# Performance work log

Measured on AMD Instinct MI355X. Metric: run time of the kernel, lower is better.

The kernel has to match this reference:

```python
import jax, jax.numpy as jnp
import numpy as np

BITS = (2, 4, 6, 8, 12, 16)
INIT_S = (0.5, 0.1, 0.05, 0.01, 0.005, 0.001)


def _round_ste(x):
    # straight-through round (LSQ)
    return x + jax.lax.stop_gradient(jnp.round(x) - x)


def _grad_scale(s, g):
    # forward = s, backward grad scaled by g (LSQ grad-scale trick)
    return s * g + jax.lax.stop_gradient(s - s * g)


def _lsq(x, s, num_bits):
    qn = -(2 ** (num_bits - 1))
    qp = 2 ** (num_bits - 1) - 1
    g = 1.0 / float(np.sqrt(x.size * qp))
    ss = _grad_scale(s, g)
    return _round_ste(jnp.clip(x / ss, qn, qp)) * ss


def _gumbel_hard(key, logits, tau):
    u = jax.random.uniform(key, logits.shape, minval=1e-10, maxval=1.0)
    gn = -jnp.log(-jnp.log(u))
    y_soft = jax.nn.softmax((logits + gn) / tau, axis=-1)
    y_hard = jax.nn.one_hot(jnp.argmax(y_soft, axis=-1), logits.shape[-1], dtype=y_soft.dtype)
    return y_hard + y_soft - jax.lax.stop_gradient(y_soft)


def setup_inputs() -> dict:
    key = jax.random.key(0)
    ks = jax.random.split(key, 16)
    B, L, N, K, HD = 64, 256, 8, 64, 64
    inp = {
        "v": jax.random.normal(ks[0], (B, L, K, 2), jnp.float32),
        "H": jax.random.normal(ks[1], (B, L, N, K, 2), jnp.float32),
        "y": jax.random.normal(ks[2], (B, L, N, 2), jnp.float32),
        "local_snr": jax.random.uniform(ks[3], (B, L, K, 1), jnp.float32),
        "w1": jax.random.normal(ks[4], (HD, 9), jnp.float32) * 0.05,
        "b1": jnp.zeros((HD,), jnp.float32),
        "w2": jax.random.normal(ks[5], (HD, HD), jnp.float32) * 0.05,
        "b2": jnp.zeros((HD,), jnp.float32),
        "w3": jax.random.normal(ks[6], (HD, HD), jnp.float32) * 0.05,
        "b3": jnp.zeros((HD,), jnp.float32),
        "wy": jax.random.normal(ks[7], (6, HD), jnp.float32) * 0.05,
        "by": jnp.zeros((6,), jnp.float32),
        "wh": jax.random.normal(ks[8], (6, HD), jnp.float32) * 0.05,
        "bh": jnp.zeros((6,), jnp.float32),
        "wd": jax.random.normal(ks[9], (6, HD), jnp.float32) * 0.05,
        "bd": jnp.zeros((6,), jnp.float32),
        "s_y": jnp.asarray(INIT_S, jnp.float32),
        "s_H": jnp.asarray(INIT_S, jnp.float32),
        "s_d": jnp.asarray(INIT_S, jnp.float32),
        "tau": 1,
    }
    return inp


def reference(v, H, y, local_snr, w1, b1, w2, b2, w3, b3, wy, by, wh, bh, wd, bd, s_y, s_H, s_d, tau):
    tau = float(tau)
    B, L, K, _ = v.shape
    N = H.shape[2]

    v_real = v[..., 0:1]
    v_imag = v[..., 1:2]
    h_power = (H ** 2).sum(axis=(2, 4))                       # (B,L,K)
    channel_norm = h_power[..., None]
    avg_channel_power = jnp.broadcast_to(h_power.mean(axis=1, keepdims=True), (B, L, K))[..., None]
    total_power = h_power.sum(axis=2, keepdims=True)          # (B,L,1)
    interference = total_power - h_power
    sir = jnp.log1p(h_power / (interference + 1e-10))[..., None]
    total_power_norm = jnp.broadcast_to(jnp.log1p(total_power), (B, L, K))[..., None]
    y_power_per_ap = (y ** 2).sum(axis=(2, 3))                # (B,L)
    y_power = jnp.broadcast_to(jnp.log1p(y_power_per_ap)[:, :, None, None], (B, L, K, 1))
    signal_power = jnp.sqrt(v_real ** 2 + v_imag ** 2 + 1e-10)

    feat = jnp.concatenate([v_real, v_imag, local_snr, channel_norm, avg_channel_power,
                            sir, total_power_norm, y_power, signal_power], axis=-1)  # (B,L,K,9)

    h = jax.nn.relu(feat @ w1.T + b1)
    h = jax.nn.relu(h @ w2.T + b2)
    h = jax.nn.relu(h @ w3.T + b3)
    logits_y = h @ wy.T + by
    logits_H = h @ wh.T + bh
    logits_d = h @ wd.T + bd

    logits_y_per_ap = logits_y.mean(axis=2)                   # (B,L,6)
    gkey = jax.random.key(42)
    g1, g2, g3 = jax.random.split(gkey, 3)
    w_y = _gumbel_hard(g1, logits_y_per_ap, tau)              # (B,L,6)
    w_H = _gumbel_hard(g2, logits_H, tau)                     # (B,L,K,6)
    w_demod = _gumbel_hard(g3, logits_d, tau)                 # (B,L,K,6)

    y_stack = jnp.stack([_lsq(y, s_y[i], BITS[i]) for i in range(6)], axis=2)   # (B,L,6,N,2)
    y_q = (y_stack * w_y[:, :, :, None, None]).sum(axis=2)

    H_stack = jnp.stack([_lsq(H, s_H[i], BITS[i]) for i in range(6)], axis=4)   # (B,L,N,K,6,2)
    H_q = (H_stack * w_H[:, :, None, :, :, None]).sum(axis=4)

    v_stack = jnp.stack([_lsq(v, s_d[i], BITS[i]) for i in range(6)], axis=3)   # (B,L,K,6,2)
    v_q = (v_stack * w_demod[..., None]).sum(axis=3)

    bit_values = jnp.asarray([2.0, 4.0, 6.0, 8.0, 12.0, 16.0], v.dtype)
    y_bits_per_ap = 2.0 * N * (w_y * bit_values).sum(axis=-1)                   # (B,L)
    y_bits_per_link = y_bits_per_ap[..., None] / K
    H_bits_per_link = 2.0 * N * (w_H * bit_values).sum(axis=-1)                 # (B,L,K)
    demod_bits_per_link = 2.0 * (w_demod * bit_values).sum(axis=-1)             # (B,L,K)
    expected_bits = y_bits_per_link + H_bits_per_link + demod_bits_per_link

    return (v_q, H_q, y_q, expected_bits, w_y, w_H, w_demod,
            y_bits_per_ap, H_bits_per_link, demod_bits_per_link)
```

## Files before the change

### kernel.cpp

```cpp
#include <hip/hip_runtime.h>
#include <cstdint>


#define JAX_PARTITIONABLE 1

constexpr int BL = 64 * 256;

constexpr long long O_vq  = 0;
constexpr long long O_Hq  = 2097152;
constexpr long long O_yq  = 18874368;
constexpr long long O_eb  = 19136512;
constexpr long long O_wy  = 20185088;
constexpr long long O_wH  = 20283392;
constexpr long long O_wd  = 26574848;
constexpr long long O_yba = 32866304;
constexpr long long O_Hbl = 32882688;
constexpr long long O_dbl = 33931264;

constexpr long long F_SAMPLE = 0;
constexpr long long F_M      = 1048576;

#define MARGIN_THETA 3e-4

__device__ __forceinline__ uint32_t rotl32(uint32_t v, int d) {
// ... 58 lines not shown
  for (int off = 32; off > 0; off >>= 1) x += __shfl_xor(x, off);
  return x;
}

__device__ __forceinline__ void argmax_gap6(const double* s, int& arg, double& gap) {
  int a = 0;
#pragma unroll
  for (int j = 1; j < 6; ++j) if (s[j] > s[a]) a = j;
  double second = -1e300;
#pragma unroll
  for (int j = 0; j < 6; ++j) if (j != a && s[j] > second) second = s[j];
  arg = a; gap = s[a] - second;
}

__device__ __forceinline__ float idx_to_bits(int i) {
  return (float)((i < 4) ? 2 * (i + 1) : (i == 4 ? 12 : 16));
}

__global__ void k0_setup(const float* __restrict__ sy, const float* __restrict__ sH,
                         const float* __restrict__ sd, float* __restrict__ ss,
                         uint32_t* __restrict__ keys) {
  const int t = threadIdx.x;
  if (t < 18) {
    const int tensor = t / 6, i = t % 6;
    const int qp_[6] = {1, 7, 31, 127, 2047, 32767};
    const long long sizes[3] = {262144LL, 16777216LL, 2097152LL};
    const float* sarr = tensor == 0 ? sy : (tensor == 1 ? sH : sd);
    const double g64 = 1.0 / sqrt((double)(sizes[tensor] * (long long)qp_[i]));
    const float g32 = (float)g64;
    const float s = sarr[i];
    const float t1 = s * g32;
    ss[t] = t1 + (s - t1);
  }
#if JAX_PARTITIONABLE
  if (t >= 32 && t < 35) {
    uint32_t o0, o1;
    threefry2x32(0u, 42u, 0u, (uint32_t)(t - 32), o0, o1);
    keys[(t - 32) * 2 + 0] = o0;
    keys[(t - 32) * 2 + 1] = o1;
  }
#else
  if (t == 32) {
    uint32_t a0, b0, a1, b1, a2, b2;
    threefry2x32(0u, 42u, 0u, 3u, a0, b0);
    threefry2x32(0u, 42u, 1u, 4u, a1, b1);
    threefry2x32(0u, 42u, 2u, 5u, a2, b2);
    keys[0] = a0; keys[1] = a1;
    keys[2] = a2; keys[3] = b0;
    keys[4] = b1; keys[5] = b2;
  }
#endif
}

__global__ __launch_bounds__(128) void k1a_hpower_partial(
    const float* __restrict__ Hm, double* __restrict__ partial) {
  const int blk = blockIdx.x;
  const int b = blk >> 3, lc = blk & 7;
  const int t = threadIdx.x;
  const float* base = Hm + (size_t)(b * 256 + lc * 32) * 1024;
  double acc = 0.0;
  for (int l = 0; l < 32; ++l) {
#pragma unroll
    for (int n = 0; n < 8; ++n) {
      const float x = base[(size_t)l * 1024 + n * 128 + t];
      acc = fma((double)x, (double)x, acc);
    }
  }
  const double other = __shfl_xor(acc, 1);
  if ((t & 1) == 0) partial[(size_t)blk * 64 + (t >> 1)] = acc + other;
}

__global__ void k1b_hpmean(const double* __restrict__ partial,
                           double* __restrict__ hp_mean) {
  const int id = blockIdx.x * blockDim.x + threadIdx.x;
  if (id >= 4096) return;
  const int b = id >> 6, k = id & 63;
  double s = 0.0;
#pragma unroll
  for (int lc = 0; lc < 8; ++lc) s += partial[(size_t)(b * 8 + lc) * 64 + k];
  hp_mean[id] = s * (1.0 / 256.0);
}

template <int NI, bool RELU>
__device__ __forceinline__ void gemm64(const float* __restrict__ inT,
                                       const float* __restrict__ WT,
                                       const float* __restrict__ bias,
                                       float* __restrict__ outT, int t) {
  const int k0 = (t & 15) * 4;
  const int j0 = (t >> 4) * 4;
  float acc[16];
#pragma unroll
  for (int jj = 0; jj < 4; ++jj) {
    const float bj = bias[j0 + jj];
#pragma unroll
    for (int kk = 0; kk < 4; ++kk) acc[jj * 4 + kk] = bj;
  }
#pragma unroll 16
  for (int i = 0; i < NI; ++i) {
    const float4 x  = *(const float4*)&inT[i * 68 + k0];
    const float4 wv = *(const float4*)&WT[i * 64 + j0];
    acc[0]  = fmaf(wv.x, x.x, acc[0]);
    acc[1]  = fmaf(wv.x, x.y, acc[1]);
    acc[2]  = fmaf(wv.x, x.z, acc[2]);
    acc[3]  = fmaf(wv.x, x.w, acc[3]);
    acc[4]  = fmaf(wv.y, x.x, acc[4]);
    acc[5]  = fmaf(wv.y, x.y, acc[5]);
    acc[6]  = fmaf(wv.y, x.z, acc[6]);
    acc[7]  = fmaf(wv.y, x.w, acc[7]);
    acc[8]  = fmaf(wv.z, x.x, acc[8]);
    acc[9]  = fmaf(wv.z, x.y, acc[9]);
    acc[10] = fmaf(wv.z, x.z, acc[10]);
    acc[11] = fmaf(wv.z, x.w, acc[11]);
    acc[12] = fmaf(wv.w, x.x, acc[12]);
    acc[13] = fmaf(wv.w, x.y, acc[13]);
    acc[14] = fmaf(wv.w, x.z, acc[14]);
    acc[15] = fmaf(wv.w, x.w, acc[15]);
  }
#pragma unroll
  for (int jj = 0; jj < 4; ++jj) {
    float4 r;
    r.x = acc[jj * 4 + 0];
    r.y = acc[jj * 4 + 1];
    r.z = acc[jj * 4 + 2];
    r.w = acc[jj * 4 + 3];
    if (RELU) {
      r.x = fmaxf(r.x, 0.0f); r.y = fmaxf(r.y, 0.0f);
      r.z = fmaxf(r.z, 0.0f); r.w = fmaxf(r.w, 0.0f);
    }
    *(float4*)&outT[(j0 + jj) * 68 + k0] = r;
  }
}

template <int NI>
__device__ __forceinline__ void gemm64_f64(const double* __restrict__ inT,
                                           const float* __restrict__ WT,
                                           const float* __restrict__ bias,
                                           double* __restrict__ outT, int t) {
  const int k0 = (t & 15) * 4;
  const int j0 = (t >> 4) * 4;
  double acc[16];
#pragma unroll
  for (int jj = 0; jj < 4; ++jj) {
    const double bj = (double)bias[j0 + jj];
#pragma unroll
    for (int kk = 0; kk < 4; ++kk) acc[jj * 4 + kk] = bj;
  }
#pragma unroll 8
  for (int i = 0; i < NI; ++i) {
    const double x0 = inT[i * 68 + k0 + 0];
    const double x1 = inT[i * 68 + k0 + 1];
    const double x2 = inT[i * 68 + k0 + 2];
    const double x3 = inT[i * 68 + k0 + 3];
    const float4 wf = *(const float4*)&WT[i * 64 + j0];
    const double w0 = (double)wf.x, w1 = (double)wf.y;
    const double w2 = (double)wf.z, w3 = (double)wf.w;
    acc[0]  = fma(w0, x0, acc[0]);
    acc[1]  = fma(w0, x1, acc[1]);
    acc[2]  = fma(w0, x2, acc[2]);
    acc[3]  = fma(w0, x3, acc[3]);
    acc[4]  = fma(w1, x0, acc[4]);
    acc[5]  = fma(w1, x1, acc[5]);
    acc[6]  = fma(w1, x2, acc[6]);
    acc[7]  = fma(w1, x3, acc[7]);
    acc[8]  = fma(w2, x0, acc[8]);
    acc[9]  = fma(w2, x1, acc[9]);
    acc[10] = fma(w2, x2, acc[10]);
    acc[11] = fma(w2, x3, acc[11]);
    acc[12] = fma(w3, x0, acc[12]);
    acc[13] = fma(w3, x1, acc[13]);
    acc[14] = fma(w3, x2, acc[14]);
    acc[15] = fma(w3, x3, acc[15]);
  }
#pragma unroll
  for (int jj = 0; jj < 4; ++jj) {
#pragma unroll
    for (int kk = 0; kk < 4; ++kk) {
      const double a = acc[jj * 4 + kk];
      outT[(j0 + jj) * 68 + k0 + kk] = a > 0.0 ? a : 0.0;
    }
  }
}

__device__ __forceinline__ void heads20(const float* __restrict__ actT,
                                        const float* __restrict__ whT,
                                        const float* __restrict__ by,
                                        const float* __restrict__ bh,
                                        const float* __restrict__ bd,
                                        float* __restrict__ headP, int t) {
  const int k = t & 63, w = t >> 6;
  float acc[5];
#pragma unroll
  for (int q = 0; q < 5; ++q) {
    const int r = w + 4 * q;
    acc[q] = (r < 6) ? by[r] : (r < 12) ? bh[r - 6] : (r < 18) ? bd[r - 12] : 0.0f;
  }
#pragma unroll 8
  for (int i = 0; i < 64; ++i) {
    const float x = actT[i * 68 + k];
#pragma unroll
    for (int q = 0; q < 5; ++q)
      acc[q] = fmaf(x, whT[(w + 4 * q) * 64 + i], acc[q]);
  }
#pragma unroll
  for (int q = 0; q < 5; ++q) {
    const int r = w + 4 * q;
    if (r < 18) headP[k * 20 + r] = acc[q];
  }
}

__device__ __forceinline__ void heads20_f64(const double* __restrict__ actT,
                                            const float* __restrict__ whT,
                                            const float* __restrict__ by,
                                            const float* __restrict__ bh,
                                            const float* __restrict__ bd,
                                            double* __restrict__ headP, int t) {
  const int k = t & 63, w = t >> 6;
  double acc[5];
#pragma unroll
  for (int q = 0; q < 5; ++q) {
    const int r = w + 4 * q;
    acc[q] = (r < 6) ? (double)by[r]
           : (r < 12) ? (double)bh[r - 6]
           : (r < 18) ? (double)bd[r - 12] : 0.0;
  }
#pragma unroll 8
  for (int i = 0; i < 64; ++i) {
    const double x = actT[i * 68 + k];
#pragma unroll
    for (int q = 0; q < 5; ++q)
      acc[q] = fma(x, (double)whT[(w + 4 * q) * 64 + i], acc[q]);
  }
#pragma unroll
  for (int q = 0; q < 5; ++q) {
    const int r = w + 4 * q;
    if (r < 18) headP[k * 20 + r] = acc[q];
  }
}

__global__ __launch_bounds__(256, 2) void k2_main(
    const float* __restrict__ v, const float* __restrict__ Hm,
    const float* __restrict__ y, const float* __restrict__ snr,
    const float* __restrict__ w1, const float* __restrict__ b1,
    const float* __restrict__ w2, const float* __restrict__ b2,
    const float* __restrict__ w3, const float* __restrict__ b3,
    const float* __restrict__ wy, const float* __restrict__ by,
    const float* __restrict__ wh, const float* __restrict__ bh,
    const float* __restrict__ wd, const float* __restrict__ bd,
    const double* __restrict__ hp_mean, const uint32_t* __restrict__ keys,
    float* __restrict__ out) {
  const int t = threadIdx.x;
  const int lane = t & 63;
  const int wvx = t >> 6;
  const int m0 = blockIdx.x * 4;

  __shared__ __align__(16) float smem[20032];
  float* w1T   = smem;
  float* w2T   = smem + 576;
  float* w3T   = smem + 4672;
  float* whT   = smem + 8768;
  float* actA  = smem + 10048;
  float* actB  = smem + 14400;
  float* headP = smem + 18752;
  double* hp4  = (double*)actB;

  for (int idx = t; idx < 576; idx += 256) {
    const int i = idx >> 6, j = idx & 63;
    w1T[idx] = w1[j * 9 + i];
  }
  for (int idx = t; idx < 4096; idx += 256) {
    const int i = idx >> 6, j = idx & 63;
    w2T[idx] = w2[j * 64 + i];
    w3T[idx] = w3[j * 64 + i];
  }
  for (int idx = t; idx < 1280; idx += 256) {
    const int r = idx >> 6, i = idx & 63;
    whT[idx] = (r < 6) ? wy[r * 64 + i]
             : (r < 12) ? wh[(r - 6) * 64 + i]
             : (r < 18) ? wd[(r - 12) * 64 + i] : 0.0f;
  }

  float ly[6], lh[6], ld[6];
#pragma unroll 1
  for (int mc = 0; mc < 4; ++mc) {
    const int m = m0 + mc;
    {
      const float2* Hp = (const float2*)Hm + (size_t)m * 512;
      double acc = 0.0;
#pragma unroll
      for (int nn = 0; nn < 2; ++nn) {
        const float2 h2v = Hp[(2 * wvx + nn) * 64 + lane];
        acc = fma((double)h2v.x, (double)h2v.x, acc);
        acc = fma((double)h2v.y, (double)h2v.y, acc);
      }
      __syncthreads();
      hp4[wvx * 64 + lane] = acc;
    }
    __syncthreads();

    if (wvx == mc) {
      const double hp = ((hp4[lane] + hp4[64 + lane]) + hp4[128 + lane]) + hp4[192 + lane];
      const double tp = wave_sum_f64(hp);
      double ypart = 0.0;
      if (lane < 16) { const double yv = (double)y[m * 16 + lane]; ypart = yv * yv; }
      const double yp = wave_sum_f64(ypart);
      const float2 vv = ((const float2*)v)[m * 64 + lane];
      const float snrv = snr[m * 64 + lane];
      const double hpm = hp_mean[(m >> 8) * 64 + lane];
      float f[9];
      f[0] = (float)vv.x;
      f[1] = (float)vv.y;
      f[2] = snrv;
      f[3] = (float)hp;
      f[4] = (float)hpm;
      f[5] = (float)log1p(hp / ((tp - hp) + 1e-10));
      f[6] = (float)log1p(tp);
      f[7] = (float)log1p(yp);
      f[8] = (float)sqrt(fma((double)vv.x, (double)vv.x,
                             fma((double)vv.y, (double)vv.y, 1e-10)));
#pragma unroll
      for (int i = 0; i < 9; ++i) actA[i * 68 + lane] = f[i];
    }
    __syncthreads();

    gemm64<9, true>(actA, w1T, b1, actB, t);
    __syncthreads();
    gemm64<64, true>(actB, w2T, b2, actA, t);
    __syncthreads();
    gemm64<64, true>(actA, w3T, b3, actB, t);
    __syncthreads();
    heads20(actB, whT, by, bh, bd, headP, t);
    __syncthreads();

    if (wvx == mc) {
#pragma unroll
      for (int j = 0; j < 6; ++j) {
        ly[j] = headP[lane * 20 + j];
        lh[j] = headP[lane * 20 + 6 + j];
        ld[j] = headP[lane * 20 + 12 + j];
      }
    }
  }

  const int m = m0 + wvx;
  const int k = lane;

  const uint32_t g1k0 = keys[0], g1k1 = keys[1];
  const uint32_t g2k0 = keys[2], g2k1 = keys[3];
  const uint32_t g3k0 = keys[4], g3k1 = keys[5];

  double sH[6], sD[6];
  const uint32_t eH = (uint32_t)(m * 64 + k) * 6u;
#pragma unroll
  for (int j = 0; j < 6; ++j) {
    const float u = bits_to_unif(jax_randbits(g2k0, g2k1, eH + j, 6291456u));
    sH[j] = (double)lh[j] + (double)(-logf(-logf(u)));
  }
#pragma unroll
  for (int j = 0; j < 6; ++j) {
    const float u = bits_to_unif(jax_randbits(g3k0, g3k1, eH + j, 6291456u));
    sD[j] = (double)ld[j] + (double)(-logf(-logf(u)));
  }
  int argH, argD; double gapH, gapD;
  argmax_gap6(sH, argH, gapH);
  argmax_gap6(sD, argD, gapD);

  double lysum[6];
#pragma unroll
  for (int j = 0; j < 6; ++j) lysum[j] = wave_sum_f64((double)ly[j]);

  int argY = 0; double gapY = 1e30;
  if (k == 0) {
    double sY[6];
#pragma unroll
    for (int j = 0; j < 6; ++j) {
      const float u = bits_to_unif(jax_randbits(g1k0, g1k1, (uint32_t)(m * 6 + j), 98304u));
      sY[j] = lysum[j] * (1.0 / 64.0) - log(-log((double)u));
    }
    argmax_gap6(sY, argY, gapY);
  }
  const int needY = __shfl((k == 0 && gapY < MARGIN_THETA) ? 1 : 0, 0);
  const bool fH = gapH < MARGIN_THETA;
  const bool fD = gapD < MARGIN_THETA;

  uint8_t* flags = (uint8_t*)(out + O_vq);
  flags[F_SAMPLE + (size_t)m * 64 + k] = (uint8_t)((fH ? 1 : 0) | (fD ? 2 : 0));
  const bool anyHD = __ballot(fH || fD) != 0ull;
  if (k == 0)
    flags[F_M + m] = (uint8_t)(((anyHD || needY) ? 1 : 0) | (needY ? 2 : 0));

  argY = __shfl(argY, 0);

  const float bY = 16.0f * idx_to_bits(argY);
  const float bH = 16.0f * idx_to_bits(argH);
  const float bD = 2.0f * idx_to_bits(argD);

  if (k == 0) {
    out[O_yba + m] = bY;
#pragma unroll
    for (int j = 0; j < 6; ++j) out[O_wy + m * 6 + j] = (j == argY) ? 1.0f : 0.0f;
  }
  out[O_Hbl + (size_t)m * 64 + k] = bH;
  out[O_dbl + (size_t)m * 64 + k] = bD;
  out[O_eb + (size_t)m * 64 + k] = (bY * 0.015625f + bH) + bD;
#pragma unroll
  for (int j = 0; j < 6; ++j) {
    out[O_wH + (size_t)(m * 64 + k) * 6 + j] = (j == argH) ? 1.0f : 0.0f;
    out[O_wd + (size_t)(m * 64 + k) * 6 + j] = (j == argD) ? 1.0f : 0.0f;
  }
}

__global__ __launch_bounds__(256, 1) void kfix(
    const float* __restrict__ v, const float* __restrict__ Hm,
    const float* __restrict__ y, const float* __restrict__ snr,
    const float* __restrict__ w1, const float* __restrict__ b1,
    const float* __restrict__ w2, const float* __restrict__ b2,
    const float* __restrict__ w3, const float* __restrict__ b3,
    const float* __restrict__ wy, const float* __restrict__ by,
    const float* __restrict__ wh, const float* __restrict__ bh,
    const float* __restrict__ wd, const float* __restrict__ bd,
    const double* __restrict__ hp_mean, const uint32_t* __restrict__ keys,
    float* __restrict__ out) {
  const int t = threadIdx.x;
  const int lane = t & 63;
  const int wvx = t >> 6;
  const int m0 = blockIdx.x * 8;
  const uint8_t* flags = (const uint8_t*)(out + O_vq);

  __shared__ uint32_t mfs[8];
  __shared__ __align__(32) char smem[120064];
  float*  w1T     = (float*)smem;
  float*  w2T     = (float*)(smem + 2304);
  float*  w3T     = (float*)(smem + 18688);
  float*  whT     = (float*)(smem + 35072);
  double* actA64  = (double*)(smem + 40192);
  double* actB64  = (double*)(smem + 75008);
  double* headP64 = (double*)(smem + 109824);
  double* hp4     = actB64;

  if (t < 8) mfs[t] = flags[F_M + m0 + t];
  __syncthreads();
  bool any = false;
#pragma unroll
  for (int i = 0; i < 8; ++i) any |= (mfs[i] != 0);
  if (!any) return;

  for (int idx = t; idx < 576; idx += 256) {
    const int i = idx >> 6, j = idx & 63;
    w1T[idx] = w1[j * 9 + i];
  }
  for (int idx = t; idx < 4096; idx += 256) {
    const int i = idx >> 6, j = idx & 63;
    w2T[idx] = w2[j * 64 + i];
    w3T[idx] = w3[j * 64 + i];
  }
  for (int idx = t; idx < 1280; idx += 256) {
    const int r = idx >> 6, i = idx & 63;
    whT[idx] = (r < 6) ? wy[r * 64 + i]
             : (r < 12) ? wh[(r - 6) * 64 + i]
             : (r < 18) ? wd[(r - 12) * 64 + i] : 0.0f;
  }
// ... 174 lines not shown
  float2 o;
  o.x = lsq1(x.x, ssv, qn, qp);
  o.y = lsq1(x.y, ssv, qn, qp);
  ((float2*)outvq)[id] = o;
}

__global__ void k5_yq(const float* __restrict__ y, const float* __restrict__ ss,
                      const float* __restrict__ ybits, float* __restrict__ outyq) {
  const int id = blockIdx.x * blockDim.x + threadIdx.x;
  if (id >= 131072) return;
  const int m = id >> 3;
  const int bits = (int)ybits[m] >> 4;
  const int i = bits_to_idx(bits);
  const float ssv = ss[i];
  const float qp = (float)((1 << (bits - 1)) - 1);
  const float qn = -(float)(1 << (bits - 1));
  const float2 x = ((const float2*)y)[id];
  float2 o;
  o.x = lsq1(x.x, ssv, qn, qp);
  o.y = lsq1(x.y, ssv, qn, qp);
  ((float2*)outyq)[id] = o;
}

extern "C" void kernel_launch(void* const* d_in, const int* in_sizes, int n_in,
                              void* d_out, int out_size, void* d_ws, size_t ws_size,
                              hipStream_t stream) {
  const float* v   = (const float*)d_in[0];
  const float* Hm  = (const float*)d_in[1];
  const float* y   = (const float*)d_in[2];
  const float* snr = (const float*)d_in[3];
  const float* w1  = (const float*)d_in[4];
  const float* b1  = (const float*)d_in[5];
  const float* w2  = (const float*)d_in[6];
  const float* b2  = (const float*)d_in[7];
  const float* w3  = (const float*)d_in[8];
  const float* b3  = (const float*)d_in[9];
  const float* wy  = (const float*)d_in[10];
  const float* by  = (const float*)d_in[11];
  const float* wh  = (const float*)d_in[12];
  const float* bh  = (const float*)d_in[13];
  const float* wd  = (const float*)d_in[14];
  const float* bd  = (const float*)d_in[15];
  const float* sy  = (const float*)d_in[16];
  const float* sH  = (const float*)d_in[17];
  const float* sd  = (const float*)d_in[18];

  float* out = (float*)d_out;

  double* ws_partial = (double*)d_ws;
  double* ws_hpmean  = ws_partial + 32768;
  float*  ws_ss      = (float*)(ws_hpmean + 4096);
  uint32_t* ws_keys  = (uint32_t*)(ws_ss + 18);

  k0_setup<<<1, 64, 0, stream>>>(sy, sH, sd, ws_ss, ws_keys);
  k1a_hpower_partial<<<512, 128, 0, stream>>>(Hm, ws_partial);
  k1b_hpmean<<<16, 256, 0, stream>>>(ws_partial, ws_hpmean);
  k2_main<<<BL / 4, 256, 0, stream>>>(v, Hm, y, snr, w1, b1, w2, b2, w3, b3,
                                      wy, by, wh, bh, wd, bd, ws_hpmean, ws_keys, out);
  kfix<<<BL / 8, 256, 0, stream>>>(v, Hm, y, snr, w1, b1, w2, b2, w3, b3,
                                   wy, by, wh, bh, wd, bd, ws_hpmean, ws_keys, out);
  k3_Hq<<<32768, 256, 0, stream>>>(Hm, ws_ss, out + O_Hbl, out + O_Hq);
  k4_vq<<<4096, 256, 0, stream>>>(v, ws_ss, out + O_dbl, out + O_vq);
  k5_yq<<<512, 256, 0, stream>>>(y, ws_ss, out + O_yba, out + O_yq);
}
```

Measured before the change: 857.6 us.

## Pre-transpose MLP weights once and run one sample per k2 block

A new small kernel transposes all MLP and head weights into a scratch area (the H_q output region, which k3 overwrites later), so k2_main no longer rebuilds a 40 KB shared-memory weight copy in every block. k2_main now handles one sample per block instead of four, reads weights from global/L2, computes each GEMM layer into registers and writes back in place to a single activation buffer. The launch bound is raised to 4 blocks per CU, cutting LDS use to about 22 KB per block. This removes redundant per-block weight staging and improves occupancy, at the cost of 4x more blocks, weight reads through cache instead of LDS, and three idle waves during the tail sampling stage.

```diff
diff --git a/kernel.cpp b/kernel.cpp
--- a/kernel.cpp
+++ b/kernel.cpp
@@ -134,6 +134,25 @@
 #endif
 }
 
+__global__ void k0w_transpose(const float* __restrict__ w1, const float* __restrict__ w2,
+                              const float* __restrict__ w3, const float* __restrict__ wy,
+                              const float* __restrict__ wh, const float* __restrict__ wd,
+                              float* __restrict__ wsT) {
+  const int t = blockIdx.x * blockDim.x + threadIdx.x;
+  for (int idx = t; idx < 576; idx += 4096)
+    wsT[idx] = w1[(idx & 63) * 9 + (idx >> 6)];
+  for (int idx = t; idx < 4096; idx += 4096) {
+    wsT[576 + idx]  = w2[(idx & 63) * 64 + (idx >> 6)];
+    wsT[4672 + idx] = w3[(idx & 63) * 64 + (idx >> 6)];
+  }
+  for (int idx = t; idx < 1280; idx += 4096) {
+    const int r = idx >> 6, i = idx & 63;
+    wsT[8768 + idx] = (r < 6) ? wy[r * 64 + i]
+                    : (r < 12) ? wh[(r - 6) * 64 + i]
+                    : (r < 18) ? wd[(r - 12) * 64 + i] : 0.0f;
+  }
+}
+
 __global__ __launch_bounds__(128) void k1a_hpower_partial(
     const float* __restrict__ Hm, double* __restrict__ partial) {
   const int blk = blockIdx.x;
@@ -163,14 +182,13 @@
   hp_mean[id] = s * (1.0 / 256.0);
 }
 
-template <int NI, bool RELU>
-__device__ __forceinline__ void gemm64(const float* __restrict__ inT,
-                                       const float* __restrict__ WT,
-                                       const float* __restrict__ bias,
-                                       float* __restrict__ outT, int t) {
+template <int NI>
+__device__ __forceinline__ void gemm_acc(const float* inT,
+                                         const float* __restrict__ WT,
+                                         const float* __restrict__ bias,
+                                         float* acc, int t) {
   const int k0 = (t & 15) * 4;
   const int j0 = (t >> 4) * 4;
-  float acc[16];
 #pragma unroll
   for (int jj = 0; jj < 4; ++jj) {
     const float bj = bias[j0 + jj];
@@ -198,18 +216,202 @@
     acc[14] = fmaf(wv.w, x.z, acc[14]);
     acc[15] = fmaf(wv.w, x.w, acc[15]);
   }
+}
+
+__device__ __forceinline__ void gemm_store(const float* acc, float* outT, int t) {
+  const int k0 = (t & 15) * 4;
+  const int j0 = (t >> 4) * 4;
 #pragma unroll
   for (int jj = 0; jj < 4; ++jj) {
     float4 r;
-    r.x = acc[jj * 4 + 0];
-    r.y = acc[jj * 4 + 1];
-    r.z = acc[jj * 4 + 2];
-    r.w = acc[jj * 4 + 3];
-    if (RELU) {
-      r.x = fmaxf(r.x, 0.0f); r.y = fmaxf(r.y, 0.0f);
-      r.z = fmaxf(r.z, 0.0f); r.w = fmaxf(r.w, 0.0f);
+    r.x = fmaxf(acc[jj * 4 + 0], 0.0f);
+    r.y = fmaxf(acc[jj * 4 + 1], 0.0f);
+    r.z = fmaxf(acc[jj * 4 + 2], 0.0f);
+    r.w = fmaxf(acc[jj * 4 + 3], 0.0f);
+    *(float4*)&outT[(j0 + jj) * 68 + k0] = r;
+  }
+}
+
+__device__ __forceinline__ void heads20(const float* actT,
+                                        const float* __restrict__ whT,
+                                        const float* __restrict__ by,
+                                        const float* __restrict__ bh,
+                                        const float* __restrict__ bd,
+                                        float* headP, int t) {
+  const int k = t & 63, w = t >> 6;
+  float acc[5];
+#pragma unroll
+  for (int q = 0; q < 5; ++q) {
+    const int r = w + 4 * q;
+    acc[q] = (r < 6) ? by[r] : (r < 12) ? bh[r - 6] : (r < 18) ? bd[r - 12] : 0.0f;
+  }
+#pragma unroll 8
+  for (int i = 0; i < 64; ++i) {
+    const float x = actT[i * 68 + k];
+#pragma unroll
+    for (int q = 0; q < 5; ++q)
+      acc[q] = fmaf(x, whT[(w + 4 * q) * 64 + i], acc[q]);
+  }
+#pragma unroll
+  for (int q = 0; q < 5; ++q) {
+    const int r = w + 4 * q;
+    if (r < 18) headP[k * 20 + r] = acc[q];
+  }
+}
+
+__global__ __launch_bounds__(256, 4) void k2_main(
+    const float* __restrict__ v, const float* __restrict__ Hm,
+    const float* __restrict__ y, const float* __restrict__ snr,
+    const float* __restrict__ b1, const float* __restrict__ b2,
+    const float* __restrict__ b3, const float* __restrict__ by,
+    const float* __restrict__ bh, const float* __restrict__ bd,
+    const float* __restrict__ wsT, const double* __restrict__ hp_mean,
+    const uint32_t* __restrict__ keys, float* __restrict__ out) {
+  const int t = threadIdx.x;
+  const int lane = t & 63;
+  const int wvx = t >> 6;
+  const int m = blockIdx.x;
+
+  __shared__ __align__(16) float smem[5632];
+  float* act   = smem;
+  float* headP = smem + 4352;
+  double* hp4  = (double*)headP;
+
+  {
+    const float2* Hp = (const float2*)Hm + (size_t)m * 512;
+    double acc = 0.0;
+#pragma unroll
+    for (int nn = 0; nn < 2; ++nn) {
+      const float2 h2v = Hp[(2 * wvx + nn) * 64 + lane];
+      acc = fma((double)h2v.x, (double)h2v.x, acc);
+      acc = fma((double)h2v.y, (double)h2v.y, acc);
     }
-    *(float4*)&outT[(j0 + jj) * 68 + k0] = r;
+    hp4[wvx * 64 + lane] = acc;
+  }
+  __syncthreads();
+
+  if (wvx == 0) {
+    const double hp = ((hp4[lane] + hp4[64 + lane]) + hp4[128 + lane]) + hp4[192 + lane];
+    const double tp = wave_sum_f64(hp);
+    double ypart = 0.0;
+    if (lane < 16) { const double yv = (double)y[m * 16 + lane]; ypart = yv * yv; }
+    const double yp = wave_sum_f64(ypart);
+    const float2 vv = ((const float2*)v)[m * 64 + lane];
+    const float snrv = snr[m * 64 + lane];
+    const double hpm = hp_mean[(m >> 8) * 64 + lane];
+    float f[9];
+    f[0] = (float)vv.x;
+    f[1] = (float)vv.y;
+    f[2] = snrv;
+    f[3] = (float)hp;
+    f[4] = (float)hpm;
+    f[5] = (float)log1p(hp / ((tp - hp) + 1e-10));
+    f[6] = (float)log1p(tp);
+    f[7] = (float)log1p(yp);
+    f[8] = (float)sqrt(fma((double)vv.x, (double)vv.x,
+                           fma((double)vv.y, (double)vv.y, 1e-10)));
+#pragma unroll
+    for (int i = 0; i < 9; ++i) act[i * 68 + lane] = f[i];
+  }
+  __syncthreads();
+
+  {
+    float a1[16];
+    gemm_acc<9>(act, wsT, b1, a1, t);
+    __syncthreads();
+    gemm_store(a1, act, t);
+  }
+  __syncthreads();
+  {
+    float a2[16];
+    gemm_acc<64>(act, wsT + 576, b2, a2, t);
+    __syncthreads();
+    gemm_store(a2, act, t);
+  }
+  __syncthreads();
+  {
+    float a3[16];
+    gemm_acc<64>(act, wsT + 4672, b3, a3, t);
+    __syncthreads();
+    gemm_store(a3, act, t);
+  }
+  __syncthreads();
+  heads20(act, wsT + 8768, by, bh, bd, headP, t);
+  __syncthreads();
+
+  if (wvx != 0) return;
+
+  const int k = lane;
+  float ly[6], lh[6], ld[6];
+#pragma unroll
+  for (int j = 0; j < 6; ++j) {
+    ly[j] = headP[k * 20 + j];
+    lh[j] = headP[k * 20 + 6 + j];
+    ld[j] = headP[k * 20 + 12 + j];
+  }
+
+  const uint32_t g1k0 = keys[0], g1k1 = keys[1];
+  const uint32_t g2k0 = keys[2], g2k1 = keys[3];
+  const uint32_t g3k0 = keys[4], g3k1 = keys[5];
+
+  double sH[6], sD[6];
+  const uint32_t eH = (uint32_t)(m * 64 + k) * 6u;
+#pragma unroll
+  for (int j = 0; j < 6; ++j) {
+    const float u = bits_to_unif(jax_randbits(g2k0, g2k1, eH + j, 6291456u));
+    sH[j] = (double)lh[j] + (double)(-logf(-logf(u)));
+  }
+#pragma unroll
+  for (int j = 0; j < 6; ++j) {
+    const float u = bits_to_unif(jax_randbits(g3k0, g3k1, eH + j, 6291456u));
+    sD[j] = (double)ld[j] + (double)(-logf(-logf(u)));
+  }
+  int argH, argD; double gapH, gapD;
+  argmax_gap6(sH, argH, gapH);
+  argmax_gap6(sD, argD, gapD);
+
+  double lysum[6];
+#pragma unroll
+  for (int j = 0; j < 6; ++j) lysum[j] = wave_sum_f64((double)ly[j]);
+
+  int argY = 0; double gapY = 1e30;
+  if (k == 0) {
+    double sY[6];
+#pragma unroll
+    for (int j = 0; j < 6; ++j) {
+      const float u = bits_to_unif(jax_randbits(g1k0, g1k1, (uint32_t)(m * 6 + j), 98304u));
+      sY[j] = lysum[j] * (1.0 / 64.0) - log(-log((double)u));
+    }
+    argmax_gap6(sY, argY, gapY);
+  }
+  const int needY = __shfl((k == 0 && gapY < MARGIN_THETA) ? 1 : 0, 0);
+  const bool fH = gapH < MARGIN_THETA;
+  const bool fD = gapD < MARGIN_THETA;
+
+  uint8_t* flags = (uint8_t*)(out + O_vq);
+  flags[F_SAMPLE + (size_t)m * 64 + k] = (uint8_t)((fH ? 1 : 0) | (fD ? 2 : 0));
+  const bool anyHD = __ballot(fH || fD) != 0ull;
+  if (k == 0)
+    flags[F_M + m] = (uint8_t)(((anyHD || needY) ? 1 : 0) | (needY ? 2 : 0));
+
+  argY = __shfl(argY, 0);
+
+  const float bY = 16.0f * idx_to_bits(argY);
+  const float bH = 16.0f * idx_to_bits(argH);
+  const float bD = 2.0f * idx_to_bits(argD);
+
+  if (k == 0) {
+    out[O_yba + m] = bY;
+#pragma unroll
+    for (int j = 0; j < 6; ++j) out[O_wy + m * 6 + j] = (j == argY) ? 1.0f : 0.0f;
+  }
+  out[O_Hbl + (size_t)m * 64 + k] = bH;
+  out[O_dbl + (size_t)m * 64 + k] = bD;
+  out[O_eb + (size_t)m * 64 + k] = (bY * 0.015625f + bH) + bD;
+#pragma unroll
+  for (int j = 0; j < 6; ++j) {
+    out[O_wH + (size_t)(m * 64 + k) * 6 + j] = (j == argH) ? 1.0f : 0.0f;
+    out[O_wd + (size_t)(m * 64 + k) * 6 + j] = (j == argD) ? 1.0f : 0.0f;
   }
 }
 
@@ -263,33 +465,6 @@
   }
 }
 
-__device__ __forceinline__ void heads20(const float* __restrict__ actT,
-                                        const float* __restrict__ whT,
-                                        const float* __restrict__ by,
-                                        const float* __restrict__ bh,
-                                        const float* __restrict__ bd,
-                                        float* __restrict__ headP, int t) {
-  const int k = t & 63, w = t >> 6;
-  float acc[5];
-#pragma unroll
-  for (int q = 0; q < 5; ++q) {
-    const int r = w + 4 * q;
-    acc[q] = (r < 6) ? by[r] : (r < 12) ? bh[r - 6] : (r < 18) ? bd[r - 12] : 0.0f;
-  }
-#pragma unroll 8
-  for (int i = 0; i < 64; ++i) {
-    const float x = actT[i * 68 + k];
-#pragma unroll
-    for (int q = 0; q < 5; ++q)
-      acc[q] = fmaf(x, whT[(w + 4 * q) * 64 + i], acc[q]);
-  }
-#pragma unroll
-  for (int q = 0; q < 5; ++q) {
-    const int r = w + 4 * q;
-    if (r < 18) headP[k * 20 + r] = acc[q];
-  }
-}
-
 __device__ __forceinline__ void heads20_f64(const double* __restrict__ actT,
                                             const float* __restrict__ whT,
                                             const float* __restrict__ by,
@@ -316,178 +491,6 @@
   for (int q = 0; q < 5; ++q) {
     const int r = w + 4 * q;
     if (r < 18) headP[k * 20 + r] = acc[q];
-  }
-}
-
-__global__ __launch_bounds__(256, 2) void k2_main(
-    const float* __restrict__ v, const float* __restrict__ Hm,
-    const float* __restrict__ y, const float* __restrict__ snr,
-    const float* __restrict__ w1, const float* __restrict__ b1,
-    const float* __restrict__ w2, const float* __restrict__ b2,
-    const float* __restrict__ w3, const float* __restrict__ b3,
-    const float* __restrict__ wy, const float* __restrict__ by,
-    const float* __restrict__ wh, const float* __restrict__ bh,
-    const float* __restrict__ wd, const float* __restrict__ bd,
-    const double* __restrict__ hp_mean, const uint32_t* __restrict__ keys,
-    float* __restrict__ out) {
-  const int t = threadIdx.x;
-  const int lane = t & 63;
-  const int wvx = t >> 6;
-  const int m0 = blockIdx.x * 4;
-
-  __shared__ __align__(16) float smem[20032];
-  float* w1T   = smem;
-  float* w2T   = smem + 576;
-  float* w3T   = smem + 4672;
-  float* whT   = smem + 8768;
-  float* actA  = smem + 10048;
-  float* actB  = smem + 14400;
-  float* headP = smem + 18752;
-  double* hp4  = (double*)actB;
-
-  for (int idx = t; idx < 576; idx += 256) {
-    const int i = idx >> 6, j = idx & 63;
-    w1T[idx] = w1[j * 9 + i];
-  }
-  for (int idx = t; idx < 4096; idx += 256) {
-    const int i = idx >> 6, j = idx & 63;
-    w2T[idx] = w2[j * 64 + i];
-    w3T[idx] = w3[j * 64 + i];
-  }
-  for (int idx = t; idx < 1280; idx += 256) {
-    const int r = idx >> 6, i = idx & 63;
-    whT[idx] = (r < 6) ? wy[r * 64 + i]
-             : (r < 12) ? wh[(r - 6) * 64 + i]
-             : (r < 18) ? wd[(r - 12) * 64 + i] : 0.0f;
-  }
-
-  float ly[6], lh[6], ld[6];
-#pragma unroll 1
-  for (int mc = 0; mc < 4; ++mc) {
-    const int m = m0 + mc;
-    {
-      const float2* Hp = (const float2*)Hm + (size_t)m * 512;
-      double acc = 0.0;
-#pragma unroll
-      for (int nn = 0; nn < 2; ++nn) {
-        const float2 h2v = Hp[(2 * wvx + nn) * 64 + lane];
-        acc = fma((double)h2v.x, (double)h2v.x, acc);
-        acc = fma((double)h2v.y, (double)h2v.y, acc);
-      }
-      __syncthreads();
-      hp4[wvx * 64 + lane] = acc;
-    }
-    __syncthreads();
-
-    if (wvx == mc) {
-      const double hp = ((hp4[lane] + hp4[64 + lane]) + hp4[128 + lane]) + hp4[192 + lane];
-      const double tp = wave_sum_f64(hp);
-      double ypart = 0.0;
-      if (lane < 16) { const double yv = (double)y[m * 16 + lane]; ypart = yv * yv; }
-      const double yp = wave_sum_f64(ypart);
-      const float2 vv = ((const float2*)v)[m * 64 + lane];
-      const float snrv = snr[m * 64 + lane];
-      const double hpm = hp_mean[(m >> 8) * 64 + lane];
-      float f[9];
-      f[0] = (float)vv.x;
-      f[1] = (float)vv.y;
-      f[2] = snrv;
-      f[3] = (float)hp;
-      f[4] = (float)hpm;
-      f[5] = (float)log1p(hp / ((tp - hp) + 1e-10));
-      f[6] = (float)log1p(tp);
-      f[7] = (float)log1p(yp);
-      f[8] = (float)sqrt(fma((double)vv.x, (double)vv.x,
-                             fma((double)vv.y, (double)vv.y, 1e-10)));
-#pragma unroll
-      for (int i = 0; i < 9; ++i) actA[i * 68 + lane] = f[i];
-    }
-    __syncthreads();
-
-    gemm64<9, true>(actA, w1T, b1, actB, t);
-    __syncthreads();
-    gemm64<64, true>(actB, w2T, b2, actA, t);
-    __syncthreads();
-    gemm64<64, true>(actA, w3T, b3, actB, t);
-    __syncthreads();
-    heads20(actB, whT, by, bh, bd, headP, t);
-    __syncthreads();
-
-    if (wvx == mc) {
-#pragma unroll
-      for (int j = 0; j < 6; ++j) {
-        ly[j] = headP[lane * 20 + j];
-        lh[j] = headP[lane * 20 + 6 + j];
-        ld[j] = headP[lane * 20 + 12 + j];
-      }
-    }
-  }
-
-  const int m = m0 + wvx;
-  const int k = lane;
-
-  const uint32_t g1k0 = keys[0], g1k1 = keys[1];
-  const uint32_t g2k0 = keys[2], g2k1 = keys[3];
-  const uint32_t g3k0 = keys[4], g3k1 = keys[5];
-
-  double sH[6], sD[6];
-  const uint32_t eH = (uint32_t)(m * 64 + k) * 6u;
-#pragma unroll
-  for (int j = 0; j < 6; ++j) {
-    const float u = bits_to_unif(jax_randbits(g2k0, g2k1, eH + j, 6291456u));
-    sH[j] = (double)lh[j] + (double)(-logf(-logf(u)));
-  }
-#pragma unroll
-  for (int j = 0; j < 6; ++j) {
-    const float u = bits_to_unif(jax_randbits(g3k0, g3k1, eH + j, 6291456u));
-    sD[j] = (double)ld[j] + (double)(-logf(-logf(u)));
-  }
-  int argH, argD; double gapH, gapD;
-  argmax_gap6(sH, argH, gapH);
-  argmax_gap6(sD, argD, gapD);
-
-  double lysum[6];
-#pragma unroll
-  for (int j = 0; j < 6; ++j) lysum[j] = wave_sum_f64((double)ly[j]);
-
-  int argY = 0; double gapY = 1e30;
-  if (k == 0) {
-    double sY[6];
-#pragma unroll
-    for (int j = 0; j < 6; ++j) {
-      const float u = bits_to_unif(jax_randbits(g1k0, g1k1, (uint32_t)(m * 6 + j), 98304u));
-      sY[j] = lysum[j] * (1.0 / 64.0) - log(-log((double)u));
-    }
-    argmax_gap6(sY, argY, gapY);
-  }
-  const int needY = __shfl((k == 0 && gapY < MARGIN_THETA) ? 1 : 0, 0);
-  const bool fH = gapH < MARGIN_THETA;
-  const bool fD = gapD < MARGIN_THETA;
-
-  uint8_t* flags = (uint8_t*)(out + O_vq);
-  flags[F_SAMPLE + (size_t)m * 64 + k] = (uint8_t)((fH ? 1 : 0) | (fD ? 2 : 0));
-  const bool anyHD = __ballot(fH || fD) != 0ull;
-  if (k == 0)
-    flags[F_M + m] = (uint8_t)(((anyHD || needY) ? 1 : 0) | (needY ? 2 : 0));
-
-  argY = __shfl(argY, 0);
-
-  const float bY = 16.0f * idx_to_bits(argY);
-  const float bH = 16.0f * idx_to_bits(argH);
-  const float bD = 2.0f * idx_to_bits(argD);
-
-  if (k == 0) {
-    out[O_yba + m] = bY;
-#pragma unroll
-    for (int j = 0; j < 6; ++j) out[O_wy + m * 6 + j] = (j == argY) ? 1.0f : 0.0f;
-  }
-  out[O_Hbl + (size_t)m * 64 + k] = bH;
-  out[O_dbl + (size_t)m * 64 + k] = bD;
-  out[O_eb + (size_t)m * 64 + k] = (bY * 0.015625f + bH) + bD;
-#pragma unroll
-  for (int j = 0; j < 6; ++j) {
-    out[O_wH + (size_t)(m * 64 + k) * 6 + j] = (j == argH) ? 1.0f : 0.0f;
-    out[O_wd + (size_t)(m * 64 + k) * 6 + j] = (j == argD) ? 1.0f : 0.0f;
   }
 }
 
@@ -768,11 +771,14 @@
   float*  ws_ss      = (float*)(ws_hpmean + 4096);
   uint32_t* ws_keys  = (uint32_t*)(ws_ss + 18);
 
+  float* wsT = out + O_Hq;
+
   k0_setup<<<1, 64, 0, stream>>>(sy, sH, sd, ws_ss, ws_keys);
+  k0w_transpose<<<16, 256, 0, stream>>>(w1, w2, w3, wy, wh, wd, wsT);
   k1a_hpower_partial<<<512, 128, 0, stream>>>(Hm, ws_partial);
   k1b_hpmean<<<16, 256, 0, stream>>>(ws_partial, ws_hpmean);
-  k2_main<<<BL / 4, 256, 0, stream>>>(v, Hm, y, snr, w1, b1, w2, b2, w3, b3,
-                                      wy, by, wh, bh, wd, bd, ws_hpmean, ws_keys, out);
+  k2_main<<<BL, 256, 0, stream>>>(v, Hm, y, snr, b1, b2, b3, by, bh, bd,
+                                  wsT, ws_hpmean, ws_keys, out);
   kfix<<<BL / 8, 256, 0, stream>>>(v, Hm, y, snr, w1, b1, w2, b2, w3, b3,
                                    wy, by, wh, bh, wd, bd, ws_hpmean, ws_keys, out);
   k3_Hq<<<32768, 256, 0, stream>>>(Hm, ws_ss, out + O_Hbl, out + O_Hq);
```

Measured after the change: 945.1 us. 1.1x slower.

## Restructure MLP kernel to one wave per sample with register-resident activations

Applied to the files above, without the earlier changes.

The main MLP kernel now launches one 64-thread block per (b,l) sample instead of 256-thread blocks that looped over four samples. Each lane keeps its whole activation vector in registers and reads weights straight from global memory as wave-uniform scalar loads. A small shared buffer is used only to transpose each layer's output back into registers. This removes the per-block weight staging into LDS and most of the __syncthreads barriers, at the cost of many more blocks, high register pressure (64-float arrays) and repeated weight reads that rely on cache hits.

```diff
diff --git a/kernel.cpp b/kernel.cpp
--- a/kernel.cpp
+++ b/kernel.cpp
@@ -163,53 +163,186 @@
   hp_mean[id] = s * (1.0 / 256.0);
 }
 
-template <int NI, bool RELU>
-__device__ __forceinline__ void gemm64(const float* __restrict__ inT,
-                                       const float* __restrict__ WT,
-                                       const float* __restrict__ bias,
-                                       float* __restrict__ outT, int t) {
-  const int k0 = (t & 15) * 4;
-  const int j0 = (t >> 4) * 4;
-  float acc[16];
-#pragma unroll
-  for (int jj = 0; jj < 4; ++jj) {
-    const float bj = bias[j0 + jj];
-#pragma unroll
-    for (int kk = 0; kk < 4; ++kk) acc[jj * 4 + kk] = bj;
-  }
-#pragma unroll 16
-  for (int i = 0; i < NI; ++i) {
-    const float4 x  = *(const float4*)&inT[i * 68 + k0];
-    const float4 wv = *(const float4*)&WT[i * 64 + j0];
-    acc[0]  = fmaf(wv.x, x.x, acc[0]);
-    acc[1]  = fmaf(wv.x, x.y, acc[1]);
-    acc[2]  = fmaf(wv.x, x.z, acc[2]);
-    acc[3]  = fmaf(wv.x, x.w, acc[3]);
-    acc[4]  = fmaf(wv.y, x.x, acc[4]);
-    acc[5]  = fmaf(wv.y, x.y, acc[5]);
-    acc[6]  = fmaf(wv.y, x.z, acc[6]);
-    acc[7]  = fmaf(wv.y, x.w, acc[7]);
-    acc[8]  = fmaf(wv.z, x.x, acc[8]);
-    acc[9]  = fmaf(wv.z, x.y, acc[9]);
-    acc[10] = fmaf(wv.z, x.z, acc[10]);
-    acc[11] = fmaf(wv.z, x.w, acc[11]);
-    acc[12] = fmaf(wv.w, x.x, acc[12]);
-    acc[13] = fmaf(wv.w, x.y, acc[13]);
-    acc[14] = fmaf(wv.w, x.z, acc[14]);
-    acc[15] = fmaf(wv.w, x.w, acc[15]);
-  }
-#pragma unroll
-  for (int jj = 0; jj < 4; ++jj) {
-    float4 r;
-    r.x = acc[jj * 4 + 0];
-    r.y = acc[jj * 4 + 1];
-    r.z = acc[jj * 4 + 2];
-    r.w = acc[jj * 4 + 3];
-    if (RELU) {
-      r.x = fmaxf(r.x, 0.0f); r.y = fmaxf(r.y, 0.0f);
-      r.z = fmaxf(r.z, 0.0f); r.w = fmaxf(r.w, 0.0f);
+__device__ __forceinline__ void layer64(const float (&hin)[64],
+                                        const float* __restrict__ W,
+                                        const float* __restrict__ bias,
+                                        float* __restrict__ hbuf, int lane) {
+#pragma unroll 1
+  for (int jg = 0; jg < 8; ++jg) {
+    float a[8];
+#pragma unroll
+    for (int q = 0; q < 8; ++q) a[q] = bias[jg * 8 + q];
+#pragma unroll
+    for (int i = 0; i < 64; ++i) {
+      const float hi = hin[i];
+#pragma unroll
+      for (int q = 0; q < 8; ++q)
+        a[q] = fmaf(W[(jg * 8 + q) * 64 + i], hi, a[q]);
     }
-    *(float4*)&outT[(j0 + jj) * 68 + k0] = r;
+#pragma unroll
+    for (int q = 0; q < 8; ++q)
+      hbuf[(jg * 8 + q) * 64 + lane] = fmaxf(a[q], 0.0f);
+  }
+  asm volatile("" ::: "memory");
+}
+
+__global__ __launch_bounds__(64) void k2_main(
+    const float* __restrict__ v, const float* __restrict__ Hm,
+    const float* __restrict__ y, const float* __restrict__ snr,
+    const float* __restrict__ w1, const float* __restrict__ b1,
+    const float* __restrict__ w2, const float* __restrict__ b2,
+    const float* __restrict__ w3, const float* __restrict__ b3,
+    const float* __restrict__ wy, const float* __restrict__ by,
+    const float* __restrict__ wh, const float* __restrict__ bh,
+    const float* __restrict__ wd, const float* __restrict__ bd,
+    const double* __restrict__ hp_mean, const uint32_t* __restrict__ keys,
+    float* __restrict__ out) {
+  const int lane = threadIdx.x;
+  const int m = blockIdx.x;
+
+  __shared__ __align__(16) float hbuf[4096];
+
+  float f[9];
+  {
+    const float2* Hp = (const float2*)Hm + (size_t)m * 512;
+    double aw[4];
+#pragma unroll
+    for (int w = 0; w < 4; ++w) {
+      double acc = 0.0;
+#pragma unroll
+      for (int nn = 0; nn < 2; ++nn) {
+        const float2 h2v = Hp[(2 * w + nn) * 64 + lane];
+        acc = fma((double)h2v.x, (double)h2v.x, acc);
+        acc = fma((double)h2v.y, (double)h2v.y, acc);
+      }
+      aw[w] = acc;
+    }
+    const double hp = ((aw[0] + aw[1]) + aw[2]) + aw[3];
+    const double tp = wave_sum_f64(hp);
+    double ypart = 0.0;
+    if (lane < 16) { const double yv = (double)y[m * 16 + lane]; ypart = yv * yv; }
+    const double yp = wave_sum_f64(ypart);
+    const float2 vv = ((const float2*)v)[m * 64 + lane];
+    const float snrv = snr[m * 64 + lane];
+    const double hpm = hp_mean[(m >> 8) * 64 + lane];
+    f[0] = (float)vv.x;
+    f[1] = (float)vv.y;
+    f[2] = snrv;
+    f[3] = (float)hp;
+    f[4] = (float)hpm;
+    f[5] = (float)log1p(hp / ((tp - hp) + 1e-10));
+    f[6] = (float)log1p(tp);
+    f[7] = (float)log1p(yp);
+    f[8] = (float)sqrt(fma((double)vv.x, (double)vv.x,
+                           fma((double)vv.y, (double)vv.y, 1e-10)));
+  }
+
+  float h1[64];
+#pragma unroll
+  for (int j = 0; j < 64; ++j) {
+    float a = b1[j];
+#pragma unroll
+    for (int i = 0; i < 9; ++i) a = fmaf(w1[j * 9 + i], f[i], a);
+    h1[j] = fmaxf(a, 0.0f);
+  }
+
+  layer64(h1, w2, b2, hbuf, lane);
+  float h2[64];
+#pragma unroll
+  for (int i = 0; i < 64; ++i) h2[i] = hbuf[i * 64 + lane];
+
+  layer64(h2, w3, b3, hbuf, lane);
+  float h3[64];
+#pragma unroll
+  for (int i = 0; i < 64; ++i) h3[i] = hbuf[i * 64 + lane];
+
+  float ly[6], lh[6], ld[6];
+#pragma unroll
+  for (int r = 0; r < 6; ++r) {
+    float a = by[r];
+#pragma unroll
+    for (int i = 0; i < 64; ++i) a = fmaf(h3[i], wy[r * 64 + i], a);
+    ly[r] = a;
+  }
+#pragma unroll
+  for (int r = 0; r < 6; ++r) {
+    float a = bh[r];
+#pragma unroll
+    for (int i = 0; i < 64; ++i) a = fmaf(h3[i], wh[r * 64 + i], a);
+    lh[r] = a;
+  }
+#pragma unroll
+  for (int r = 0; r < 6; ++r) {
+    float a = bd[r];
+#pragma unroll
+    for (int i = 0; i < 64; ++i) a = fmaf(h3[i], wd[r * 64 + i], a);
+    ld[r] = a;
+  }
+
+  const int k = lane;
+
+  const uint32_t g1k0 = keys[0], g1k1 = keys[1];
+  const uint32_t g2k0 = keys[2], g2k1 = keys[3];
+  const uint32_t g3k0 = keys[4], g3k1 = keys[5];
+
+  double sH[6], sD[6];
+  const uint32_t eH = (uint32_t)(m * 64 + k) * 6u;
+#pragma unroll
+  for (int j = 0; j < 6; ++j) {
+    const float u = bits_to_unif(jax_randbits(g2k0, g2k1, eH + j, 6291456u));
+    sH[j] = (double)lh[j] + (double)(-logf(-logf(u)));
+  }
+#pragma unroll
+  for (int j = 0; j < 6; ++j) {
+    const float u = bits_to_unif(jax_randbits(g3k0, g3k1, eH + j, 6291456u));
+    sD[j] = (double)ld[j] + (double)(-logf(-logf(u)));
+  }
+  int argH, argD; double gapH, gapD;
+  argmax_gap6(sH, argH, gapH);
+  argmax_gap6(sD, argD, gapD);
+
+  double lysum[6];
+#pragma unroll
+  for (int j = 0; j < 6; ++j) lysum[j] = wave_sum_f64((double)ly[j]);
+
+  int argY = 0; double gapY = 1e30;
+  if (k == 0) {
+    double sY[6];
+#pragma unroll
+    for (int j = 0; j < 6; ++j) {
+      const float u = bits_to_unif(jax_randbits(g1k0, g1k1, (uint32_t)(m * 6 + j), 98304u));
+      sY[j] = lysum[j] * (1.0 / 64.0) - log(-log((double)u));
+    }
+    argmax_gap6(sY, argY, gapY);
+  }
+  const int needY = __shfl((k == 0 && gapY < MARGIN_THETA) ? 1 : 0, 0);
+  const bool fH = gapH < MARGIN_THETA;
+  const bool fD = gapD < MARGIN_THETA;
+
+  uint8_t* flags = (uint8_t*)(out + O_vq);
+  flags[F_SAMPLE + (size_t)m * 64 + k] = (uint8_t)((fH ? 1 : 0) | (fD ? 2 : 0));
+  const bool anyHD = __ballot(fH || fD) != 0ull;
+  if (k == 0)
+    flags[F_M + m] = (uint8_t)(((anyHD || needY) ? 1 : 0) | (needY ? 2 : 0));
+
+  argY = __shfl(argY, 0);
+
+  const float bY = 16.0f * idx_to_bits(argY);
+  const float bH = 16.0f * idx_to_bits(argH);
+  const float bD = 2.0f * idx_to_bits(argD);
+
+  if (k == 0) {
+    out[O_yba + m] = bY;
+#pragma unroll
+    for (int j = 0; j < 6; ++j) out[O_wy + m * 6 + j] = (j == argY) ? 1.0f : 0.0f;
+  }
+  out[O_Hbl + (size_t)m * 64 + k] = bH;
+  out[O_dbl + (size_t)m * 64 + k] = bD;
+  out[O_eb + (size_t)m * 64 + k] = (bY * 0.015625f + bH) + bD;
+#pragma unroll
+  for (int j = 0; j < 6; ++j) {
+    out[O_wH + (size_t)(m * 64 + k) * 6 + j] = (j == argH) ? 1.0f : 0.0f;
+    out[O_wd + (size_t)(m * 64 + k) * 6 + j] = (j == argD) ? 1.0f : 0.0f;
   }
 }
 
@@ -263,33 +396,6 @@
   }
 }
 
-__device__ __forceinline__ void heads20(const float* __restrict__ actT,
-                                        const float* __restrict__ whT,
-                                        const float* __restrict__ by,
-                                        const float* __restrict__ bh,
-                                        const float* __restrict__ bd,
-                                        float* __restrict__ headP, int t) {
-  const int k = t & 63, w = t >> 6;
-  float acc[5];
-#pragma unroll
-  for (int q = 0; q < 5; ++q) {
-    const int r = w + 4 * q;
-    acc[q] = (r < 6) ? by[r] : (r < 12) ? bh[r - 6] : (r < 18) ? bd[r - 12] : 0.0f;
-  }
-#pragma unroll 8
-  for (int i = 0; i < 64; ++i) {
-    const float x = actT[i * 68 + k];
-#pragma unroll
-    for (int q = 0; q < 5; ++q)
-      acc[q] = fmaf(x, whT[(w + 4 * q) * 64 + i], acc[q]);
-  }
-#pragma unroll
-  for (int q = 0; q < 5; ++q) {
-    const int r = w + 4 * q;
-    if (r < 18) headP[k * 20 + r] = acc[q];
-  }
-}
-
 __device__ __forceinline__ void heads20_f64(const double* __restrict__ actT,
                                             const float* __restrict__ whT,
                                             const float* __restrict__ by,
@@ -316,178 +422,6 @@
   for (int q = 0; q < 5; ++q) {
     const int r = w + 4 * q;
     if (r < 18) headP[k * 20 + r] = acc[q];
-  }
-}
-
-__global__ __launch_bounds__(256, 2) void k2_main(
-    const float* __restrict__ v, const float* __restrict__ Hm,
-    const float* __restrict__ y, const float* __restrict__ snr,
-    const float* __restrict__ w1, const float* __restrict__ b1,
-    const float* __restrict__ w2, const float* __restrict__ b2,
-    const float* __restrict__ w3, const float* __restrict__ b3,
-    const float* __restrict__ wy, const float* __restrict__ by,
-    const float* __restrict__ wh, const float* __restrict__ bh,
-    const float* __restrict__ wd, const float* __restrict__ bd,
-    const double* __restrict__ hp_mean, const uint32_t* __restrict__ keys,
-    float* __restrict__ out) {
-  const int t = threadIdx.x;
-  const int lane = t & 63;
-  const int wvx = t >> 6;
-  const int m0 = blockIdx.x * 4;
-
-  __shared__ __align__(16) float smem[20032];
-  float* w1T   = smem;
-  float* w2T   = smem + 576;
-  float* w3T   = smem + 4672;
-  float* whT   = smem + 8768;
-  float* actA  = smem + 10048;
-  float* actB  = smem + 14400;
-  float* headP = smem + 18752;
-  double* hp4  = (double*)actB;
-
-  for (int idx = t; idx < 576; idx += 256) {
-    const int i = idx >> 6, j = idx & 63;
-    w1T[idx] = w1[j * 9 + i];
-  }
-  for (int idx = t; idx < 4096; idx += 256) {
-    const int i = idx >> 6, j = idx & 63;
-    w2T[idx] = w2[j * 64 + i];
-    w3T[idx] = w3[j * 64 + i];
-  }
-  for (int idx = t; idx < 1280; idx += 256) {
-    const int r = idx >> 6, i = idx & 63;
-    whT[idx] = (r < 6) ? wy[r * 64 + i]
-             : (r < 12) ? wh[(r - 6) * 64 + i]
-             : (r < 18) ? wd[(r - 12) * 64 + i] : 0.0f;
-  }
-
-  float ly[6], lh[6], ld[6];
-#pragma unroll 1
-  for (int mc = 0; mc < 4; ++mc) {
-    const int m = m0 + mc;
-    {
-      const float2* Hp = (const float2*)Hm + (size_t)m * 512;
-      double acc = 0.0;
-#pragma unroll
-      for (int nn = 0; nn < 2; ++nn) {
-        const float2 h2v = Hp[(2 * wvx + nn) * 64 + lane];
-        acc = fma((double)h2v.x, (double)h2v.x, acc);
-        acc = fma((double)h2v.y, (double)h2v.y, acc);
-      }
-      __syncthreads();
-      hp4[wvx * 64 + lane] = acc;
-    }
-    __syncthreads();
-
-    if (wvx == mc) {
-      const double hp = ((hp4[lane] + hp4[64 + lane]) + hp4[128 + lane]) + hp4[192 + lane];
-      const double tp = wave_sum_f64(hp);
-      double ypart = 0.0;
-      if (lane < 16) { const double yv = (double)y[m * 16 + lane]; ypart = yv * yv; }
-      const double yp = wave_sum_f64(ypart);
-      const float2 vv = ((const float2*)v)[m * 64 + lane];
-      const float snrv = snr[m * 64 + lane];
-      const double hpm = hp_mean[(m >> 8) * 64 + lane];
-      float f[9];
-      f[0] = (float)vv.x;
-      f[1] = (float)vv.y;
-      f[2] = snrv;
-      f[3] = (float)hp;
-      f[4] = (float)hpm;
-      f[5] = (float)log1p(hp / ((tp - hp) + 1e-10));
-      f[6] = (float)log1p(tp);
-      f[7] = (float)log1p(yp);
-      f[8] = (float)sqrt(fma((double)vv.x, (double)vv.x,
-                             fma((double)vv.y, (double)vv.y, 1e-10)));
-#pragma unroll
-      for (int i = 0; i < 9; ++i) actA[i * 68 + lane] = f[i];
-    }
-    __syncthreads();
-
-    gemm64<9, true>(actA, w1T, b1, actB, t);
-    __syncthreads();
-    gemm64<64, true>(actB, w2T, b2, actA, t);
-    __syncthreads();
-    gemm64<64, true>(actA, w3T, b3, actB, t);
-    __syncthreads();
-    heads20(actB, whT, by, bh, bd, headP, t);
-    __syncthreads();
-
-    if (wvx == mc) {
-#pragma unroll
-      for (int j = 0; j < 6; ++j) {
-        ly[j] = headP[lane * 20 + j];
-        lh[j] = headP[lane * 20 + 6 + j];
-        ld[j] = headP[lane * 20 + 12 + j];
-      }
-    }
-  }
-
-  const int m = m0 + wvx;
-  const int k = lane;
-
-  const uint32_t g1k0 = keys[0], g1k1 = keys[1];
-  const uint32_t g2k0 = keys[2], g2k1 = keys[3];
-  const uint32_t g3k0 = keys[4], g3k1 = keys[5];
-
-  double sH[6], sD[6];
-  const uint32_t eH = (uint32_t)(m * 64 + k) * 6u;
-#pragma unroll
-  for (int j = 0; j < 6; ++j) {
-    const float u = bits_to_unif(jax_randbits(g2k0, g2k1, eH + j, 6291456u));
-    sH[j] = (double)lh[j] + (double)(-logf(-logf(u)));
-  }
-#pragma unroll
-  for (int j = 0; j < 6; ++j) {
-    const float u = bits_to_unif(jax_randbits(g3k0, g3k1, eH + j, 6291456u));
-    sD[j] = (double)ld[j] + (double)(-logf(-logf(u)));
-  }
-  int argH, argD; double gapH, gapD;
-  argmax_gap6(sH, argH, gapH);
-  argmax_gap6(sD, argD, gapD);
-
-  double lysum[6];
-#pragma unroll
-  for (int j = 0; j < 6; ++j) lysum[j] = wave_sum_f64((double)ly[j]);
-
-  int argY = 0; double gapY = 1e30;
-  if (k == 0) {
-    double sY[6];
-#pragma unroll
-    for (int j = 0; j < 6; ++j) {
-      const float u = bits_to_unif(jax_randbits(g1k0, g1k1, (uint32_t)(m * 6 + j), 98304u));
-      sY[j] = lysum[j] * (1.0 / 64.0) - log(-log((double)u));
-    }
-    argmax_gap6(sY, argY, gapY);
-  }
-  const int needY = __shfl((k == 0 && gapY < MARGIN_THETA) ? 1 : 0, 0);
-  const bool fH = gapH < MARGIN_THETA;
-  const bool fD = gapD < MARGIN_THETA;
-
-  uint8_t* flags = (uint8_t*)(out + O_vq);
-  flags[F_SAMPLE + (size_t)m * 64 + k] = (uint8_t)((fH ? 1 : 0) | (fD ? 2 : 0));
-  const bool anyHD = __ballot(fH || fD) != 0ull;
-  if (k == 0)
-    flags[F_M + m] = (uint8_t)(((anyHD || needY) ? 1 : 0) | (needY ? 2 : 0));
-
-  argY = __shfl(argY, 0);
-
-  const float bY = 16.0f * idx_to_bits(argY);
-  const float bH = 16.0f * idx_to_bits(argH);
-  const float bD = 2.0f * idx_to_bits(argD);
-
-  if (k == 0) {
-    out[O_yba + m] = bY;
-#pragma unroll
-    for (int j = 0; j < 6; ++j) out[O_wy + m * 6 + j] = (j == argY) ? 1.0f : 0.0f;
-  }
-  out[O_Hbl + (size_t)m * 64 + k] = bH;
-  out[O_dbl + (size_t)m * 64 + k] = bD;
-  out[O_eb + (size_t)m * 64 + k] = (bY * 0.015625f + bH) + bD;
-#pragma unroll
-  for (int j = 0; j < 6; ++j) {
-    out[O_wH + (size_t)(m * 64 + k) * 6 + j] = (j == argH) ? 1.0f : 0.0f;
-    out[O_wd + (size_t)(m * 64 + k) * 6 + j] = (j == argD) ? 1.0f : 0.0f;
   }
 }
 
@@ -771,8 +705,8 @@
   k0_setup<<<1, 64, 0, stream>>>(sy, sH, sd, ws_ss, ws_keys);
   k1a_hpower_partial<<<512, 128, 0, stream>>>(Hm, ws_partial);
   k1b_hpmean<<<16, 256, 0, stream>>>(ws_partial, ws_hpmean);
-  k2_main<<<BL / 4, 256, 0, stream>>>(v, Hm, y, snr, w1, b1, w2, b2, w3, b3,
-                                      wy, by, wh, bh, wd, bd, ws_hpmean, ws_keys, out);
+  k2_main<<<BL, 64, 0, stream>>>(v, Hm, y, snr, w1, b1, w2, b2, w3, b3,
+                                 wy, by, wh, bh, wd, bd, ws_hpmean, ws_keys, out);
   kfix<<<BL / 8, 256, 0, stream>>>(v, Hm, y, snr, w1, b1, w2, b2, w3, b3,
                                    wy, by, wh, bh, wd, bd, ws_hpmean, ws_keys, out);
   k3_Hq<<<32768, 256, 0, stream>>>(Hm, ws_ss, out + O_Hbl, out + O_Hq);
```

Result: slower. 907.2 us (+5.8%).
